# Kernel optimization log

Measured on AMD Instinct MI355X. Metric: run time of the kernel, lower is better.

Reference implementation:

```python
import jax, jax.numpy as jnp
import numpy as np

NUM_LEVELS = 16
MIN_RES = 16
GROWTH = 1.38
TABLE_SZ = 16384
# Per-level resolutions computed in float64 like torch's python-float b**level
RESOLUTIONS = jnp.asarray(np.floor(MIN_RES * GROWTH ** np.arange(NUM_LEVELS)).astype(np.float32))
# Spatial-hash constants; 2654435761 wraps to int32 like torch's .int() arithmetic
H2 = np.uint32(2654435761).astype(np.int32)
H3 = np.int32(805459861)
# Corner order v0..v7 from get_nearest_vertices_coords: 1 -> use ceil, 0 -> use floor
CORNERS = np.array([[0,0,0],[1,0,0],[1,1,0],[0,1,0],[0,0,1],[1,0,1],[1,1,1],[0,1,1]], dtype=bool)


def setup_inputs() -> dict:
    key = jax.random.key(0)
    kx, kt = jax.random.split(key)
    x = jax.random.uniform(kx, (262144, 3), dtype=jnp.float32)
    # original init: uniform(-1e-4, 1e-4); small-scale random values
    tables = jax.random.normal(kt, (NUM_LEVELS, TABLE_SZ, 2), dtype=jnp.float32) * 1e-4
    return {"x": x, "tables": tables}


def reference(x, tables):
    B = x.shape[0]
    F = tables.shape[-1]
    mask = jnp.asarray(CORNERS)  # [8,3]
    scaled = RESOLUTIONS[:, None, None] * x[None]        # [L,B,3]
    lo = jnp.floor(scaled).astype(jnp.int32)             # [L,B,3]
    hi = jnp.ceil(scaled).astype(jnp.int32)              # [L,B,3]
    verts = jnp.where(mask[None, None], hi[:, :, None, :], lo[:, :, None, :])  # [L,B,8,3]
    vx, vy, vz = verts[..., 0], verts[..., 1], verts[..., 2]
    # int32 spatial hash with wraparound multiply, then python-style mod (non-negative)
    idx = jnp.remainder(vx ^ (H2 * vy) ^ (H3 * vz), TABLE_SZ)  # [L,B,8]
    feats = jax.vmap(lambda t, i: t[i])(tables, idx)           # [L,B,8,F]
    # NOTE: faithful to source: interpolation weights use the UNSCALED position
    w = x - jnp.floor(x)                                       # [B,3]
    # trilinear weight per corner = prod_d (w_d if corner high else 1-w_d)
    cw = jnp.prod(jnp.where(mask[None], w[:, None, :], 1.0 - w[:, None, :]), axis=-1)  # [B,8]
    out = jnp.einsum('lbvf,bv->lbf', feats, cw)                # [L,B,F]
    return jnp.transpose(out, (1, 0, 2)).reshape(B, NUM_LEVELS * F)
```

## Files before the change

kernel.cpp:

```cpp
#include <hip/hip_runtime.h>
#include <hip/hip_fp16.h>
#include <stdint.h>


#define NUM_LEVELS 16
#define TABLE_SZ   16384
#define NCHUNK     32
#define BLOCK      512

__constant__ float RESV[NUM_LEVELS] = {
    16.f, 22.f, 30.f, 42.f, 58.f, 80.f, 110.f, 152.f,
    210.f, 290.f, 400.f, 553.f, 763.f, 1053.f, 1453.f, 2005.f
};

struct PointCtx {
    uint32_t off[8];
    float    cw[8];
};

__device__ __forceinline__ void make_ctx(float px, float py, float pz, float r,
                                         PointCtx& c)
{
    float wx = px - floorf(px);
    float wy = py - floorf(py);
    float wz = pz - floorf(pz);
    float ox = 1.f - wx, oy = 1.f - wy, oz = 1.f - wz;

    c.cw[0] = ox * oy * oz;
    c.cw[1] = wx * oy * oz;
    c.cw[2] = wx * wy * oz;
    c.cw[3] = ox * wy * oz;
    c.cw[4] = ox * oy * wz;
    c.cw[5] = wx * oy * wz;
    c.cw[6] = wx * wy * wz;
    c.cw[7] = ox * wy * wz;

    float sx = r * px, sy = r * py, sz = r * pz;
    uint32_t mxl = ((uint32_t)(int)floorf(sx) & (TABLE_SZ - 1)) << 2;
    uint32_t mxh = ((uint32_t)(int)ceilf(sx)  & (TABLE_SZ - 1)) << 2;
    uint32_t myl = ((2654435761u * (uint32_t)(int)floorf(sy)) & (TABLE_SZ - 1)) << 2;
    uint32_t myh = ((2654435761u * (uint32_t)(int)ceilf(sy))  & (TABLE_SZ - 1)) << 2;
    uint32_t mzl = ((805459861u  * (uint32_t)(int)floorf(sz)) & (TABLE_SZ - 1)) << 2;
    uint32_t mzh = ((805459861u  * (uint32_t)(int)ceilf(sz))  & (TABLE_SZ - 1)) << 2;

    c.off[0] = mxl ^ myl ^ mzl;
    c.off[1] = mxh ^ myl ^ mzl;
    c.off[2] = mxh ^ myh ^ mzl;
    c.off[3] = mxl ^ myh ^ mzl;
    c.off[4] = mxl ^ myl ^ mzh;
    c.off[5] = mxh ^ myl ^ mzh;
    c.off[6] = mxh ^ myh ^ mzh;
    c.off[7] = mxl ^ myh ^ mzh;
}

__global__ __launch_bounds__(BLOCK, 4)
void hashenc_lds_kernel(const float* __restrict__ x,
                        const float* __restrict__ tables,
                        float* __restrict__ out,
                        int B, int pts_per_block)
{
    __shared__ __half2 tab[TABLE_SZ];

    const int level = blockIdx.x >> 5;
    const int chunk = blockIdx.x & (NCHUNK - 1);

    {
        const float4* __restrict__ gt4 =
            (const float4*)(tables + (size_t)level * (TABLE_SZ * 2));
        #pragma unroll
        for (int i = threadIdx.x; i < TABLE_SZ / 2; i += BLOCK) {
            float4 v = gt4[i];
            tab[2 * i]     = __floats2half2_rn(v.x, v.y);
            tab[2 * i + 1] = __floats2half2_rn(v.z, v.w);
        }
    }
    __syncthreads();

    const float r = RESV[level];
    const char* tb = (const char*)tab;

    int b = chunk * pts_per_block + threadIdx.x;
    const int pair_iters = pts_per_block / (2 * BLOCK);

    float pxA = x[3 * b + 0],           pyA = x[3 * b + 1],           pzA = x[3 * b + 2];
    float pxB = x[3 * (b + BLOCK) + 0], pyB = x[3 * (b + BLOCK) + 1], pzB = x[3 * (b + BLOCK) + 2];

    for (int k = 0; k < pair_iters; ++k) {
        float nxA = pxA, nyA = pyA, nzA = pzA;
        float nxB = pxB, nyB = pyB, nzB = pzB;
        int nb = b + 2 * BLOCK;
        if (k + 1 < pair_iters) {
            nxA = x[3 * nb + 0];             nyA = x[3 * nb + 1];             nzA = x[3 * nb + 2];
            nxB = x[3 * (nb + BLOCK) + 0];   nyB = x[3 * (nb + BLOCK) + 1];   nzB = x[3 * (nb + BLOCK) + 2];
        }

        PointCtx cA, cB;
        make_ctx(pxA, pyA, pzA, r, cA);
        make_ctx(pxB, pyB, pzB, r, cB);

        float2 fA[8], fB[8];
        #pragma unroll
        for (int c = 0; c < 8; ++c)
            fA[c] = __half22float2(*(const __half2*)(tb + cA.off[c]));
        #pragma unroll
        for (int c = 0; c < 8; ++c)
            fB[c] = __half22float2(*(const __half2*)(tb + cB.off[c]));

        float a0 = 0.f, a1 = 0.f, b0 = 0.f, b1 = 0.f;
        #pragma unroll
        for (int c = 0; c < 8; ++c) {
            a0 += fA[c].x * cA.cw[c];
            a1 += fA[c].y * cA.cw[c];
            b0 += fB[c].x * cB.cw[c];
            b1 += fB[c].y * cB.cw[c];
        }

        ((float2*)out)[(size_t)b * NUM_LEVELS + level]           = make_float2(a0, a1);
        ((float2*)out)[(size_t)(b + BLOCK) * NUM_LEVELS + level] = make_float2(b0, b1);

        pxA = nxA; pyA = nyA; pzA = nzA;
        pxB = nxB; pyB = nyB; pzB = nzB;
        b = nb;
    }
}

extern "C" void kernel_launch(void* const* d_in, const int* in_sizes, int n_in,
                              void* d_out, int out_size, void* d_ws, size_t ws_size,
                              hipStream_t stream) {
    const float* x      = (const float*)d_in[0];
    const float* tables = (const float*)d_in[1];
    float* out          = (float*)d_out;
    int B = in_sizes[0] / 3;
    int pts_per_block = (B + NCHUNK - 1) / NCHUNK;
    dim3 grid(NUM_LEVELS * NCHUNK);
    hashenc_lds_kernel<<<grid, BLOCK, 0, stream>>>(x, tables, out, B, pts_per_block);
}
```

Before: 90.69 us.

## Stage per-level results in half-precision workspace and transpose in separate kernel

The encode kernel now writes each level's two features as a contiguous half2 into a level-major workspace instead of scattered 8-byte stores into the interleaved output. A second kernel reads the workspace through shared memory and writes fully coalesced float4 rows to the output. This targets the uncoalesced strided store pattern. The cost is an extra kernel launch, an extra workspace round trip, and rounding the outputs to half precision, which changes numerics. It falls back to the old path if the workspace is too small.

Result: no change. 91.95 us (+1.4%).

```diff
diff --git a/kernel.cpp b/kernel.cpp
--- a/kernel.cpp
+++ b/kernel.cpp
@@ -7,6 +7,7 @@
 #define TABLE_SZ   16384
 #define NCHUNK     32
 #define BLOCK      512
+#define TBLOCK     256
 
 __constant__ float RESV[NUM_LEVELS] = {
     16.f, 22.f, 30.f, 42.f, 58.f, 80.f, 110.f, 152.f,
@@ -53,9 +54,11 @@
     c.off[7] = mxl ^ myh ^ mzh;
 }
 
+template<int MODE>
 __global__ __launch_bounds__(BLOCK, 4)
 void hashenc_lds_kernel(const float* __restrict__ x,
                         const float* __restrict__ tables,
+                        __half2* __restrict__ ws,
                         float* __restrict__ out,
                         int B, int pts_per_block)
 {
@@ -78,6 +81,7 @@
 
     const float r = RESV[level];
     const char* tb = (const char*)tab;
+    __half2* wsl = ws + (size_t)level * B;
 
     int b = chunk * pts_per_block + threadIdx.x;
     const int pair_iters = pts_per_block / (2 * BLOCK);
@@ -115,12 +119,42 @@
             b1 += fB[c].y * cB.cw[c];
         }
 
-        ((float2*)out)[(size_t)b * NUM_LEVELS + level]           = make_float2(a0, a1);
-        ((float2*)out)[(size_t)(b + BLOCK) * NUM_LEVELS + level] = make_float2(b0, b1);
+        if (MODE == 0) {
+            wsl[b]         = __floats2half2_rn(a0, a1);
+            wsl[b + BLOCK] = __floats2half2_rn(b0, b1);
+        } else {
+            ((float2*)out)[(size_t)b * NUM_LEVELS + level]           = make_float2(a0, a1);
+            ((float2*)out)[(size_t)(b + BLOCK) * NUM_LEVELS + level] = make_float2(b0, b1);
+        }
 
         pxA = nxA; pyA = nyA; pzA = nzA;
         pxB = nxB; pyB = nyB; pzB = nzB;
         b = nb;
+    }
+}
+
+__global__ __launch_bounds__(TBLOCK)
+void transpose_kernel(const __half2* __restrict__ ws,
+                      float* __restrict__ out, int B)
+{
+    __shared__ __half2 buf[TBLOCK][NUM_LEVELS + 1];
+    const int p0 = blockIdx.x * TBLOCK;
+    const int t  = threadIdx.x;
+
+    #pragma unroll
+    for (int l = 0; l < NUM_LEVELS; ++l)
+        buf[t][l] = ws[(size_t)l * B + p0 + t];
+    __syncthreads();
+
+    const int pl = t >> 3;
+    const int j  = t & 7;
+    float4* o = (float4*)out;
+    #pragma unroll
+    for (int i = 0; i < 8; ++i) {
+        int p = pl + i * 32;
+        float2 f0 = __half22float2(buf[p][2 * j]);
+        float2 f1 = __half22float2(buf[p][2 * j + 1]);
+        o[(size_t)(p0 + p) * 8 + j] = make_float4(f0.x, f0.y, f1.x, f1.y);
     }
 }
 
@@ -133,5 +167,13 @@
     int B = in_sizes[0] / 3;
     int pts_per_block = (B + NCHUNK - 1) / NCHUNK;
     dim3 grid(NUM_LEVELS * NCHUNK);
-    hashenc_lds_kernel<<<grid, BLOCK, 0, stream>>>(x, tables, out, B, pts_per_block);
+
+    size_t ws_needed = (size_t)NUM_LEVELS * B * sizeof(__half2);
+    if (ws_size >= ws_needed && (B % TBLOCK) == 0) {
+        __half2* ws = (__half2*)d_ws;
+        hashenc_lds_kernel<0><<<grid, BLOCK, 0, stream>>>(x, tables, ws, out, B, pts_per_block);
+        transpose_kernel<<<dim3(B / TBLOCK), TBLOCK, 0, stream>>>(ws, out, B);
+    } else {
+        hashenc_lds_kernel<1><<<grid, BLOCK, 0, stream>>>(x, tables, nullptr, out, B, pts_per_block);
+    }
 }
```
